# Performance work log

Measured on AMD Instinct MI355X. Metric: run time of the kernel, lower is better.

The kernel has to match this reference:

```python
import jax, jax.numpy as jnp
import numpy as np

OUT = 8192   # out_features
IN = 8192    # in_features
GS = 64      # HQQ group_size (axis=0 grouping)
NG = OUT * IN // GS   # number of quantization groups = 1048576
B = 64       # tokens in the batch


def setup_inputs() -> dict:
    key = jax.random.key(0)
    k1, k2, k3, k4, k5 = jax.random.split(key, 5)
    x = jax.random.normal(k1, (B, IN), dtype=jnp.float32)
    # packed 4-bit weights: two 4-bit values per byte, packed along axis 0
    # (HQQ pack_4bit_u8: packed = (W[:GS//2] << 4) | W[GS//2:])
    W_q = jax.random.randint(k2, (GS // 2, NG), 0, 256, dtype=jnp.int32)
    scale = jax.random.uniform(k3, (1, NG), dtype=jnp.float32, minval=0.001, maxval=0.02)
    zero = jax.random.uniform(k4, (1, NG), dtype=jnp.float32, minval=0.0, maxval=15.0)
    bias = jax.random.normal(k5, (OUT,), dtype=jnp.float32) * 0.01
    return {"x": x, "W_q": W_q, "scale": scale, "zero": zero, "bias": bias}


def reference(x, W_q, scale, zero, bias):
    # Unpack 4-bit: high nibble holds rows [0, GS//2), low nibble rows [GS//2, GS)
    hi = (W_q >> 4).astype(jnp.float32)          # (GS//2, NG)
    lo = (W_q & 0xF).astype(jnp.float32)         # (GS//2, NG)
    Wu = jnp.concatenate([hi, lo], axis=0)       # (GS, NG)
    # HQQ group-wise dequant: W = (W_q - zero) * scale, then reshape to (out, in)
    W = ((Wu - zero) * scale).reshape(OUT, IN)
    # linear: y = x @ W^T + bias
    return x @ W.T + bias
```

## Files before the change

### kernel.cpp

```cpp
#include <hip/hip_runtime.h>
#include <stdint.h>

#define OUT_F 8192
#define IN_F  8192
#define NGRP  1048576
#define BATCH 64
#define KS    4
#define NSTEP ((IN_F / KS) / 128)

typedef float f32x4  __attribute__((ext_vector_type(4)));
typedef float f32x16 __attribute__((ext_vector_type(16)));
typedef _Float16 half8_t __attribute__((ext_vector_type(8)));

static __device__ __forceinline__ unsigned int pk_fma_f16(unsigned int a, unsigned int b, unsigned int c) {
  unsigned int d;
  asm("v_pk_fma_f16 %0, %1, %2, %3" : "=v"(d) : "v"(a), "v"(b), "v"(c));
  return d;
}
static __device__ __forceinline__ unsigned int pk16(float a, float b) {
  unsigned short ua = __builtin_bit_cast(unsigned short, (_Float16)a);
  unsigned short ub = __builtin_bit_cast(unsigned short, (_Float16)b);
  return (unsigned int)ua | ((unsigned int)ub << 16);
}

#define GLL16(g, l)                                                         \
  __builtin_amdgcn_global_load_lds(                                         \
      (const __attribute__((address_space(1))) void*)(g),                   \
      (__attribute__((address_space(3))) void*)(l), 16, 0, 0)

__global__ __launch_bounds__(256) void pre_kernel(const float* __restrict__ x, ushort* __restrict__ xh,
                                                  const float* __restrict__ scale, const float* __restrict__ zero,
                                                  uint32_t* __restrict__ szb) {
  const int b = blockIdx.x;
  if (b < 512) {
    const int i = b * 256 + threadIdx.x;
    float4 v = ((const float4*)x)[i];
    ushort4 o;
    o.x = __builtin_bit_cast(unsigned short, (_Float16)v.x);
    o.y = __builtin_bit_cast(unsigned short, (_Float16)v.y);
    o.z = __builtin_bit_cast(unsigned short, (_Float16)v.z);
    o.w = __builtin_bit_cast(unsigned short, (_Float16)v.w);
    ((ushort4*)xh)[i] = o;
  } else {
    const int i = (b - 512) * 256 + threadIdx.x;
    float4 s = ((const float4*)scale)[i];
    float4 z = ((const float4*)zero)[i];
    uint4 o;
    o.x = pk16(s.x, s.y);
    o.y = pk16(-(64.f + z.x) * s.x, -(64.f + z.y) * s.y);
    o.z = pk16(s.z, s.w);
    o.w = pk16(-(64.f + z.z) * s.z, -(64.f + z.w) * s.w);
    ((uint4*)szb)[i] = o;
  }
}

__global__ __launch_bounds__(512, 4) void hqq_gemm_kernel(
    const int* __restrict__ Wq, const uint32_t* __restrict__ szb,
    const ushort* __restrict__ xh, float* __restrict__ part)
{
  __shared__ ushort xlds[3][64 * 128];
  __shared__ ushort blds[2][64 * 128];

  const int t    = threadIdx.x;
  const int bid  = blockIdx.x;
  const int ks   = bid & 3;
  const int c    = bid >> 2;
  const int lane = t & 63;
  const int wid  = t >> 6;
  const int kbase = ks * (IN_F / KS);

  const int lr = t >> 5;
  const int i0 = (t & 31) * 4;
  const int* __restrict__ wq0 = Wq + (size_t)lr * NGRP + (size_t)c * IN_F + kbase + i0;
  const int* __restrict__ wq1 = wq0 + (size_t)16 * NGRP;
  const uint8_t* __restrict__ szp =
      (const uint8_t*)szb + ((size_t)c * IN_F + kbase + i0) * 4;
  const int wb0 = (i0 * 2) ^ ((lr & 7) << 4);

  const int kh   = wid & 1;
  const int mh   = (wid >> 1) & 1;
  const int nh   = wid >> 2;
  const int ln31 = lane & 31;
  const int koct = lane >> 5;
  const int arow = mh * 32 + ln31;
  const int brow = nh * 32 + ln31;

  f32x16 acc = {0.f, 0.f, 0.f, 0.f, 0.f, 0.f, 0.f, 0.f,
                0.f, 0.f, 0.f, 0.f, 0.f, 0.f, 0.f, 0.f};

  auto stage_x = [&](int bi, int s) {
    #pragma unroll
    for (int j = 0; j < 2; ++j) {
      const int m    = wid * 8 + j * 4 + (lane >> 4);
      const int scol = ((lane & 15) * 16) ^ ((m & 7) << 4);
      const ushort* g = xh + (size_t)m * IN_F + kbase + s * 128 + (scol >> 1);
      GLL16(g, &xlds[bi][(wid * 8 + j * 4) * 128]);
    }
  };

  auto ldregs = [&](int s, int4& w0, int4& w1, uint4& z4) {
    w0 = *(const int4*)(wq0 + (size_t)s * 128);
    w1 = *(const int4*)(wq1 + (size_t)s * 128);
    z4 = *(const uint4*)(szp + (size_t)s * 512);
  };

  auto stage_b = [&](int bi, const int4& w0, const int4& w1, const uint4& z4) {
    uint8_t* bb = (uint8_t*)&blds[bi][0];
    auto dqrow = [&](const int4& wv, int r) {
      unsigned tt0 = ((unsigned)wv.y << 16) | (unsigned)wv.x;
      unsigned tt1 = ((unsigned)wv.w << 16) | (unsigned)wv.z;
      uint2 hh, ll;
      hh.x = pk_fma_f16((tt0 & 0x00F000F0u) | 0x54005400u, z4.x, z4.y);
      hh.y = pk_fma_f16((tt1 & 0x00F000F0u) | 0x54005400u, z4.z, z4.w);
      ll.x = pk_fma_f16(((tt0 << 4) & 0x00F000F0u) | 0x54005400u, z4.x, z4.y);
      ll.y = pk_fma_f16(((tt1 << 4) & 0x00F000F0u) | 0x54005400u, z4.z, z4.w);
      *(uint2*)(bb + r * 256 + wb0)        = hh;
      *(uint2*)(bb + (r + 32) * 256 + wb0) = ll;
    };
    dqrow(w0, lr);
    dqrow(w1, lr + 16);
  };

  {
    int4 a0, a1; uint4 z0;
    ldregs(0, a0, a1, z0);
    stage_b(0, a0, a1, z0);
  }
  stage_x(0, 0);
  stage_x(1, 1);
  int4 w0, w1; uint4 z4;
  ldregs(1, w0, w1, z4);

  int xr0 = 0, xr1 = 1, xr2 = 2;

  #pragma unroll 1
  for (int s = 0; s < NSTEP; ++s) {
    asm volatile("s_waitcnt lgkmcnt(0)" ::: "memory");
    __builtin_amdgcn_s_barrier();

    const bool more2 = (s + 2 < NSTEP);
    int4 n0, n1; uint4 nz;
    if (more2) {
      stage_x(xr2, s + 2);
      ldregs(s + 2, n0, n1, nz);
    }

    if (more2)               asm volatile("s_waitcnt vmcnt(10)" ::: "memory");
    else if (s + 1 < NSTEP)  asm volatile("s_waitcnt vmcnt(5)" ::: "memory");
    else                     asm volatile("s_waitcnt vmcnt(0)" ::: "memory");
    __builtin_amdgcn_sched_barrier(0);

    const uint8_t* xb   = (const uint8_t*)&xlds[xr0][0];
    const uint8_t* bbuf = (const uint8_t*)&blds[s & 1][0];
    #pragma unroll
    for (int j = 0; j < 4; ++j) {
      const int kk   = kh * 4 + j;
      const int colb = (kk * 16 + koct * 8) * 2;
      half8_t a = *(const half8_t*)(xb   + arow * 256 + (colb ^ ((arow & 7) << 4)));
      half8_t b = *(const half8_t*)(bbuf + brow * 256 + (colb ^ ((brow & 7) << 4)));
      acc = __builtin_amdgcn_mfma_f32_32x32x16_f16(a, b, acc, 0, 0, 0);
    }

    if (s + 1 < NSTEP) stage_b((s + 1) & 1, w0, w1, z4);
    if (more2) { w0 = n0; w1 = n1; z4 = nz; }

    const int tmp = xr0; xr0 = xr1; xr1 = xr2; xr2 = tmp;
  }

  __syncthreads();
  float* red = (float*)&blds[0][0];
  {
    float4* dst = (float4*)(red + ((size_t)(wid * 64 + lane)) * 16);
    dst[0] = (float4){acc[0],  acc[1],  acc[2],  acc[3]};
    dst[1] = (float4){acc[4],  acc[5],  acc[6],  acc[7]};
    dst[2] = (float4){acc[8],  acc[9],  acc[10], acc[11]};
    dst[3] = (float4){acc[12], acc[13], acc[14], acc[15]};
  }
  __syncthreads();
  if (kh == 0) {
    const float4* src = (const float4*)(red + ((size_t)((wid ^ 1) * 64 + lane)) * 16);
    float4 p0 = src[0], p1 = src[1], p2 = src[2], p3 = src[3];
    const int o = ln31 * 128 + c + nh * 4096;
    const int mbase = mh * 32 + 4 * koct;
    float* bp = part + ((size_t)ks * OUT_F + o) * BATCH + mbase;
    *(float4*)(bp +  0) = (float4){acc[0]  + p0.x, acc[1]  + p0.y, acc[2]  + p0.z, acc[3]  + p0.w};
    *(float4*)(bp +  8) = (float4){acc[4]  + p1.x, acc[5]  + p1.y, acc[6]  + p1.z, acc[7]  + p1.w};
    *(float4*)(bp + 16) = (float4){acc[8]  + p2.x, acc[9]  + p2.y, acc[10] + p2.z, acc[11] + p2.w};
    *(float4*)(bp + 24) = (float4){acc[12] + p3.x, acc[13] + p3.y, acc[14] + p3.z, acc[15] + p3.w};
  }
}

__global__ __launch_bounds__(256) void reduce_kernel(const float* __restrict__ part,
                                                     const float* __restrict__ bias,
                                                     float* __restrict__ out)
{
  __shared__ float tile[32][65];
  const int ob = blockIdx.x;
  const int t  = threadIdx.x;
  {
    const int ol = t >> 3;
    const int mg = t & 7;
    const int o  = ob * 32 + ol;
    const size_t base = (size_t)o * BATCH + mg * 8;
    float s[8] = {0, 0, 0, 0, 0, 0, 0, 0};
    #pragma unroll
    for (int ks = 0; ks < KS; ++ks) {
      const float* p = part + (size_t)ks * OUT_F * BATCH + base;
      float4 a = *(const float4*)p;
      float4 b = *(const float4*)(p + 4);
      s[0] += a.x; s[1] += a.y; s[2] += a.z; s[3] += a.w;
      s[4] += b.x; s[5] += b.y; s[6] += b.z; s[7] += b.w;
    }
    const float bv = bias[o];
    #pragma unroll
    for (int j = 0; j < 8; ++j) tile[ol][mg * 8 + j] = s[j] + bv;
  }
  __syncthreads();
  {
    const int m  = t >> 2;
    const int og = (t & 3) * 8;
    float r[8];
    #pragma unroll
    for (int j = 0; j < 8; ++j) r[j] = tile[og + j][m];
    float* op = out + (size_t)m * OUT_F + ob * 32 + og;
    *(float4*)op       = (float4){r[0], r[1], r[2], r[3]};
    *(float4*)(op + 4) = (float4){r[4], r[5], r[6], r[7]};
  }
}

__global__ void hqq_fallback_kernel(const float* __restrict__ x, const int* __restrict__ Wq,
                                    const float* __restrict__ scale, const float* __restrict__ zero,
                                    const float* __restrict__ bias, float* __restrict__ out)
{
  int idx = blockIdx.x * blockDim.x + threadIdx.x;
  int b = idx >> 13;
  int o = idx & 8191;
  int g = o >> 7, cc = o & 127;
  int r = g & 31;
  bool hi = (g < 32);
  const int*   wrow = Wq    + (size_t)r  * NGRP + (size_t)cc * IN_F;
  const float* srow = scale + (size_t)cc * IN_F;
  const float* zrow = zero  + (size_t)cc * IN_F;
  const float* xrow = x     + (size_t)b  * IN_F;
  float acc = 0.f;
  for (int k = 0; k < IN_F; ++k) {
    int v = wrow[k];
    float nib = (float)(hi ? (v >> 4) : (v & 15));
    acc += xrow[k] * ((nib - zrow[k]) * srow[k]);
  }
  out[idx] = acc + bias[o];
}

extern "C" void kernel_launch(void* const* d_in, const int* in_sizes, int n_in,
                              void* d_out, int out_size, void* d_ws, size_t ws_size,
                              hipStream_t stream) {
  const float* x     = (const float*)d_in[0];
  const int*   Wq    = (const int*)d_in[1];
  const float* scale = (const float*)d_in[2];
  const float* zero  = (const float*)d_in[3];
  const float* bias  = (const float*)d_in[4];
  float* out = (float*)d_out;

  const size_t xh_bytes   = (size_t)BATCH * IN_F * sizeof(ushort);
  const size_t sz_bytes   = (size_t)NGRP * 4;
  const size_t part_bytes = (size_t)KS * BATCH * OUT_F * sizeof(float);

  if (ws_size >= xh_bytes + sz_bytes + part_bytes) {
    ushort*   xh   = (ushort*)d_ws;
    uint32_t* szb  = (uint32_t*)((char*)d_ws + xh_bytes);
    float*    part = (float*)((char*)d_ws + xh_bytes + sz_bytes);
    pre_kernel<<<1536, 256, 0, stream>>>(x, xh, scale, zero, szb);
    hqq_gemm_kernel<<<128 * KS, 512, 0, stream>>>(Wq, szb, xh, part);
    reduce_kernel<<<OUT_F / 32, 256, 0, stream>>>(part, bias, out);
  } else {
    hqq_fallback_kernel<<<(BATCH * OUT_F) / 256, 256, 0, stream>>>(x, Wq, scale, zero, bias, out);
  }
}
```

Measured before the change: 40.73 us.

## Double split-K factor and halve K tile to raise block count and occupancy

```diff
diff --git a/kernel.cpp b/kernel.cpp
--- a/kernel.cpp
+++ b/kernel.cpp
@@ -5,8 +5,9 @@
 #define IN_F  8192
 #define NGRP  1048576
 #define BATCH 64
-#define KS    4
-#define NSTEP ((IN_F / KS) / 128)
+#define KS    8
+#define BK    64
+#define NSTEP ((IN_F / KS) / BK)
 
 typedef float f32x4  __attribute__((ext_vector_type(4)));
 typedef float f32x16 __attribute__((ext_vector_type(16)));
@@ -54,25 +55,24 @@
   }
 }
 
-__global__ __launch_bounds__(512, 4) void hqq_gemm_kernel(
+__global__ __launch_bounds__(512, 6) void hqq_gemm_kernel(
     const int* __restrict__ Wq, const uint32_t* __restrict__ szb,
     const ushort* __restrict__ xh, float* __restrict__ part)
 {
-  __shared__ ushort xlds[3][64 * 128];
-  __shared__ ushort blds[2][64 * 128];
+  __shared__ ushort xlds[3][64 * 64];
+  __shared__ ushort blds[2][64 * 64];
 
   const int t    = threadIdx.x;
   const int bid  = blockIdx.x;
-  const int ks   = bid & 3;
-  const int c    = bid >> 2;
+  const int ks   = bid & 7;
+  const int c    = bid >> 3;
   const int lane = t & 63;
   const int wid  = t >> 6;
   const int kbase = ks * (IN_F / KS);
 
-  const int lr = t >> 5;
-  const int i0 = (t & 31) * 4;
+  const int lr = t >> 4;
+  const int i0 = (t & 15) * 4;
   const int* __restrict__ wq0 = Wq + (size_t)lr * NGRP + (size_t)c * IN_F + kbase + i0;
-  const int* __restrict__ wq1 = wq0 + (size_t)16 * NGRP;
   const uint8_t* __restrict__ szp =
       (const uint8_t*)szb + ((size_t)c * IN_F + kbase + i0) * 4;
   const int wb0 = (i0 * 2) ^ ((lr & 7) << 4);
@@ -89,47 +89,39 @@
                 0.f, 0.f, 0.f, 0.f, 0.f, 0.f, 0.f, 0.f};
 
   auto stage_x = [&](int bi, int s) {
-    #pragma unroll
-    for (int j = 0; j < 2; ++j) {
-      const int m    = wid * 8 + j * 4 + (lane >> 4);
-      const int scol = ((lane & 15) * 16) ^ ((m & 7) << 4);
-      const ushort* g = xh + (size_t)m * IN_F + kbase + s * 128 + (scol >> 1);
-      GLL16(g, &xlds[bi][(wid * 8 + j * 4) * 128]);
-    }
+    const int m    = wid * 8 + (lane >> 3);
+    const int scol = ((lane & 7) * 16) ^ ((m & 7) << 4);
+    const ushort* g = xh + (size_t)m * IN_F + kbase + s * BK + (scol >> 1);
+    GLL16(g, &xlds[bi][(wid * 8) * 64]);
   };
 
-  auto ldregs = [&](int s, int4& w0, int4& w1, uint4& z4) {
-    w0 = *(const int4*)(wq0 + (size_t)s * 128);
-    w1 = *(const int4*)(wq1 + (size_t)s * 128);
-    z4 = *(const uint4*)(szp + (size_t)s * 512);
+  auto ldregs = [&](int s, int4& w0, uint4& z4) {
+    w0 = *(const int4*)(wq0 + (size_t)s * BK);
+    z4 = *(const uint4*)(szp + (size_t)s * (BK * 4));
   };
 
-  auto stage_b = [&](int bi, const int4& w0, const int4& w1, const uint4& z4) {
+  auto stage_b = [&](int bi, const int4& w0, const uint4& z4) {
     uint8_t* bb = (uint8_t*)&blds[bi][0];
-    auto dqrow = [&](const int4& wv, int r) {
-      unsigned tt0 = ((unsigned)wv.y << 16) | (unsigned)wv.x;
-      unsigned tt1 = ((unsigned)wv.w << 16) | (unsigned)wv.z;
-      uint2 hh, ll;
-      hh.x = pk_fma_f16((tt0 & 0x00F000F0u) | 0x54005400u, z4.x, z4.y);
-      hh.y = pk_fma_f16((tt1 & 0x00F000F0u) | 0x54005400u, z4.z, z4.w);
-      ll.x = pk_fma_f16(((tt0 << 4) & 0x00F000F0u) | 0x54005400u, z4.x, z4.y);
-      ll.y = pk_fma_f16(((tt1 << 4) & 0x00F000F0u) | 0x54005400u, z4.z, z4.w);
-      *(uint2*)(bb + r * 256 + wb0)        = hh;
-      *(uint2*)(bb + (r + 32) * 256 + wb0) = ll;
-    };
-    dqrow(w0, lr);
-    dqrow(w1, lr + 16);
+    unsigned tt0 = ((unsigned)w0.y << 16) | (unsigned)w0.x;
+    unsigned tt1 = ((unsigned)w0.w << 16) | (unsigned)w0.z;
+    uint2 hh, ll;
+    hh.x = pk_fma_f16((tt0 & 0x00F000F0u) | 0x54005400u, z4.x, z4.y);
+    hh.y = pk_fma_f16((tt1 & 0x00F000F0u) | 0x54005400u, z4.z, z4.w);
+    ll.x = pk_fma_f16(((tt0 << 4) & 0x00F000F0u) | 0x54005400u, z4.x, z4.y);
+    ll.y = pk_fma_f16(((tt1 << 4) & 0x00F000F0u) | 0x54005400u, z4.z, z4.w);
+    *(uint2*)(bb + lr * 128 + wb0)        = hh;
+    *(uint2*)(bb + (lr + 32) * 128 + wb0) = ll;
   };
 
   {
-    int4 a0, a1; uint4 z0;
-    ldregs(0, a0, a1, z0);
-    stage_b(0, a0, a1, z0);
+    int4 a0; uint4 z0;
+    ldregs(0, a0, z0);
+    stage_b(0, a0, z0);
   }
   stage_x(0, 0);
   stage_x(1, 1);
-  int4 w0, w1; uint4 z4;
-  ldregs(1, w0, w1, z4);
+  int4 w0; uint4 z4;
+  ldregs(1, w0, z4);
 
   int xr0 = 0, xr1 = 1, xr2 = 2;
 
@@ -139,36 +131,36 @@
     __builtin_amdgcn_s_barrier();
 
     const bool more2 = (s + 2 < NSTEP);
-    int4 n0, n1; uint4 nz;
+    int4 n0; uint4 nz;
     if (more2) {
       stage_x(xr2, s + 2);
-      ldregs(s + 2, n0, n1, nz);
+      ldregs(s + 2, n0, nz);
     }
 
-    if (more2)               asm volatile("s_waitcnt vmcnt(10)" ::: "memory");
-    else if (s + 1 < NSTEP)  asm volatile("s_waitcnt vmcnt(5)" ::: "memory");
+    if (more2)               asm volatile("s_waitcnt vmcnt(6)" ::: "memory");
+    else if (s + 1 < NSTEP)  asm volatile("s_waitcnt vmcnt(3)" ::: "memory");
     else                     asm volatile("s_waitcnt vmcnt(0)" ::: "memory");
     __builtin_amdgcn_sched_barrier(0);
 
     const uint8_t* xb   = (const uint8_t*)&xlds[xr0][0];
     const uint8_t* bbuf = (const uint8_t*)&blds[s & 1][0];
     #pragma unroll
-    for (int j = 0; j < 4; ++j) {
-      const int kk   = kh * 4 + j;
+    for (int j = 0; j < 2; ++j) {
+      const int kk   = kh * 2 + j;
       const int colb = (kk * 16 + koct * 8) * 2;
-      half8_t a = *(const half8_t*)(xb   + arow * 256 + (colb ^ ((arow & 7) << 4)));
-      half8_t b = *(const half8_t*)(bbuf + brow * 256 + (colb ^ ((brow & 7) << 4)));
+      half8_t a = *(const half8_t*)(xb   + arow * 128 + (colb ^ ((arow & 7) << 4)));
+      half8_t b = *(const half8_t*)(bbuf + brow * 128 + (colb ^ ((brow & 7) << 4)));
       acc = __builtin_amdgcn_mfma_f32_32x32x16_f16(a, b, acc, 0, 0, 0);
     }
 
-    if (s + 1 < NSTEP) stage_b((s + 1) & 1, w0, w1, z4);
-    if (more2) { w0 = n0; w1 = n1; z4 = nz; }
+    if (s + 1 < NSTEP) stage_b((s + 1) & 1, w0, z4);
+    if (more2) { w0 = n0; z4 = nz; }
 
     const int tmp = xr0; xr0 = xr1; xr1 = xr2; xr2 = tmp;
   }
 
   __syncthreads();
-  float* red = (float*)&blds[0][0];
+  float* red = (float*)&xlds[0][0];
   {
     float4* dst = (float4*)(red + ((size_t)(wid * 64 + lane)) * 16);
     dst[0] = (float4){acc[0],  acc[1],  acc[2],  acc[3]};
```

Measured after the change: 42.91 us. +5.4%, slower.
